# Performance work log

Measured on AMD Instinct MI355X. Metric: run time of the kernel, lower is better.

Reference implementation:

```python
import jax, jax.numpy as jnp
import numpy as np

B, C, N, K, COUT = 2, 192, 16384, 16, 192
EPS = 1e-5


def setup_inputs() -> dict:
    key = jax.random.key(0)
    k1, k2, k3 = jax.random.split(key, 3)
    x = jax.random.normal(k1, (B, C, N, 1), dtype=jnp.float32)
    edge_index = jax.random.randint(k2, (2, B, N, K), 0, N, dtype=jnp.int32)
    # kaiming-normal-ish 1x1 conv weight, flattened to [C_out, 2C]
    W = jax.random.normal(k3, (COUT, 2 * C), dtype=jnp.float32) * np.float32(np.sqrt(2.0 / (2 * C)))
    b_conv = jnp.zeros((COUT,), jnp.float32)
    gamma = jnp.ones((COUT,), jnp.float32)
    beta = jnp.zeros((COUT,), jnp.float32)
    return {"x": x, "W": W, "b_conv": b_conv, "gamma": gamma, "beta": beta, "edge_index": edge_index}


def reference(x, W, b_conv, gamma, beta, edge_index):
    b, c, n, _ = x.shape
    k = edge_index.shape[-1]
    xs = x[..., 0]  # [B,C,N]

    def gather(idx):  # idx: [B,N,K] -> [B,C,N,K]
        return jnp.take_along_axis(xs, idx.reshape(b, 1, n * k), axis=2).reshape(b, c, n, k)

    x_i = gather(edge_index[1])
    x_j = gather(edge_index[0])
    mr = jnp.max(x_j - x_i, axis=-1)  # max-relative feature [B,C,N]

    # torch.cat([x.unsqueeze(2), x_j.unsqueeze(2)], 2).reshape(b, 2c, n, 1) interleaves channels
    cat = jnp.stack([xs, mr], axis=2).reshape(b, 2 * c, n)  # [B,2C,N]

    # 1x1 conv == channel matmul
    h = jnp.einsum('oc,bcn->bon', W, cat) + b_conv[None, :, None]  # [B,COUT,N]

    # BatchNorm2d (training-mode batch statistics over batch+spatial dims)
    mean = h.mean(axis=(0, 2), keepdims=True)
    var = h.var(axis=(0, 2), keepdims=True)
    h = (h - mean) / jnp.sqrt(var + EPS) * gamma[None, :, None] + beta[None, :, None]

    out = jax.nn.gelu(h, approximate=False)
    return out[..., None]  # [B,COUT,N,1]
```

## Files before the change

### kernel.cpp

```cpp
#include <hip/hip_runtime.h>
#include <math.h>

#define BB 2
#define CC 192
#define NN 16384
#define KK 16
#define COUT 192
#define MM (BB * NN)
#define KDIM (2 * CC)
#define EPSF 1e-5f
#define NGB 256

typedef __attribute__((ext_vector_type(8))) short short8;
typedef __attribute__((ext_vector_type(4))) float f32x4;

#define AS1P const __attribute__((address_space(1))) void*
#define AS3P __attribute__((address_space(3))) void*

static __device__ __forceinline__ float bf16_to_f32(unsigned int u16) {
    return __uint_as_float(u16 << 16);
}
static __device__ __forceinline__ float bf16hi_to_f32(unsigned int u) {
    return __uint_as_float(u & 0xffff0000u);
}
static __device__ __forceinline__ unsigned short f32_to_bf16(float f) {
    unsigned int u = __float_as_uint(f);
    unsigned int r = (u + 0x7fffu + ((u >> 16) & 1u)) >> 16;
    return (unsigned short)r;
}

#define TRB (512 * 3 * BB)
__global__ __launch_bounds__(256) void k_prep(const float* __restrict__ x,
                                              unsigned int* __restrict__ xt32,
                                              const float* __restrict__ W,
                                              unsigned short* __restrict__ Wb) {
    int bid = blockIdx.x;
    int t = threadIdx.x;
    if (bid >= TRB) {
        int wb = bid - TRB;
        int base = wb * 1024 + t * 4;
        float4 v = *(const float4*)(W + base);
        uint2 o;
        o.x = (unsigned int)f32_to_bf16(v.x) | ((unsigned int)f32_to_bf16(v.y) << 16);
        o.y = (unsigned int)f32_to_bf16(v.z) | ((unsigned int)f32_to_bf16(v.w) << 16);
        *(uint2*)(Wb + base) = o;
        return;
    }
    __shared__ float tile[64][33];
    int nb = bid & 511;
    int rest = bid >> 9;
    int cb = rest % 3;
    int b = rest / 3;
    int n0 = nb * 32, c0 = cb * 64;
    int tx = t & 31, ty = t >> 5;
    #pragma unroll
    for (int j = 0; j < 64; j += 8)
        tile[ty + j][tx] = x[((size_t)b * CC + (c0 + ty + j)) * NN + n0 + tx];
    __syncthreads();
    #pragma unroll
    for (int j = 0; j < 32; j += 8) {
        int n = n0 + ty + j;
        unsigned int w = (unsigned int)f32_to_bf16(tile[2 * tx][ty + j]) |
                         ((unsigned int)f32_to_bf16(tile[2 * tx + 1][ty + j]) << 16);
        xt32[(((size_t)b * NN + n) * CC + c0) / 2 + tx] = w;
    }
}

__global__ __launch_bounds__(384) void k_gather(const unsigned short* __restrict__ xt,
                                                const int* __restrict__ edge,
                                                uint4* __restrict__ xcat4) {
    __shared__ int sj[16][KK], si[16][KK];
    int t = threadIdx.x;
    int m0 = blockIdx.x * 16;
    int b = m0 >> 14, n0 = m0 & (NN - 1);
    if (t < 256)
        ((int*)sj)[t] = edge[((size_t)b * NN + n0) * KK + t];
    if (t >= 128)
        ((int*)si)[t - 128] = edge[((size_t)(BB + b) * NN + n0) * KK + (t - 128)];
    __syncthreads();

    int p = t / 24, c4 = t % 24;
    const uint4* base = (const uint4*)(xt + (size_t)b * NN * CC) + c4;
    float mx[8];
    #pragma unroll
    for (int c = 0; c < 8; ++c) mx[c] = -INFINITY;
    #pragma unroll
    for (int k = 0; k < KK; ++k) {
        uint4 vj = base[(size_t)sj[p][k] * 24];
        uint4 vi = base[(size_t)si[p][k] * 24];
        const unsigned int dj[4] = {vj.x, vj.y, vj.z, vj.w};
        const unsigned int di[4] = {vi.x, vi.y, vi.z, vi.w};
        #pragma unroll
        for (int d = 0; d < 4; ++d) {
            mx[2 * d]     = fmaxf(mx[2 * d],     bf16_to_f32(dj[d] & 0xffffu) - bf16_to_f32(di[d] & 0xffffu));
            mx[2 * d + 1] = fmaxf(mx[2 * d + 1], bf16hi_to_f32(dj[d]) - bf16hi_to_f32(di[d]));
        }
    }
    uint4 xs = base[(size_t)(n0 + p) * 24];
    uint4 o0, o1;
    o0.x = (xs.x & 0xffffu) | ((unsigned int)f32_to_bf16(mx[0]) << 16);
    o0.y = (xs.x >> 16)     | ((unsigned int)f32_to_bf16(mx[1]) << 16);
    o0.z = (xs.y & 0xffffu) | ((unsigned int)f32_to_bf16(mx[2]) << 16);
    o0.w = (xs.y >> 16)     | ((unsigned int)f32_to_bf16(mx[3]) << 16);
    o1.x = (xs.z & 0xffffu) | ((unsigned int)f32_to_bf16(mx[4]) << 16);
    o1.y = (xs.z >> 16)     | ((unsigned int)f32_to_bf16(mx[5]) << 16);
    o1.z = (xs.w & 0xffffu) | ((unsigned int)f32_to_bf16(mx[6]) << 16);
    o1.w = (xs.w >> 16)     | ((unsigned int)f32_to_bf16(mx[7]) << 16);
    size_t orow = (size_t)(m0 + p) * 48;
    xcat4[orow + 2 * c4] = o0;
    xcat4[orow + 2 * c4 + 1] = o1;
}

#define BMT 128
__global__ __launch_bounds__(512) void k_gemm(const unsigned short* __restrict__ xcat,
                                              const unsigned short* __restrict__ Wb,
                                              unsigned short* __restrict__ h,
                                              float* __restrict__ psum,
                                              float* __restrict__ psum2) {
    __shared__ __align__(16) char ldsA[BMT * 128];
    __shared__ __align__(16) char ldsB[COUT * 128];
    int t = threadIdx.x;
    int m0 = blockIdx.x * BMT;
    int w = t >> 6, l = t & 63, lo = l & 15, q4 = l >> 4;
    int lr = l >> 3, lc = l & 7;
    f32x4 acc[12];
    #pragma unroll
    for (int i = 0; i < 12; ++i) acc[i] = (f32x4){0.f, 0.f, 0.f, 0.f};
    int rA = w * 16 + lo;

    for (int ks = 0; ks < KDIM / 64; ++ks) {
        int k0 = ks * 64;
        if (ks) __syncthreads();
        #pragma unroll
        for (int e = 0; e < 2; ++e) {
            int r = w * 16 + e * 8 + lr;
            int cg = lc ^ (r & 7);
            const unsigned short* gp = xcat + (size_t)(m0 + r) * KDIM + k0 + cg * 8;
            __builtin_amdgcn_global_load_lds((AS1P)gp, (AS3P)(ldsA + w * 2048 + e * 1024), 16, 0, 0);
        }
        #pragma unroll
        for (int e = 0; e < 3; ++e) {
            int r = w * 24 + e * 8 + lr;
            int cg = lc ^ (r & 7);
            const unsigned short* gp = Wb + (size_t)r * KDIM + k0 + cg * 8;
            __builtin_amdgcn_global_load_lds((AS1P)gp, (AS3P)(ldsB + w * 3072 + e * 1024), 16, 0, 0);
        }
        __syncthreads();
        #pragma unroll
        for (int kh = 0; kh < 2; ++kh) {
            int cb = kh * 64 + q4 * 16;
            short8 a = *(const short8*)(ldsA + rA * 128 + (cb ^ ((rA & 7) << 4)));
            #pragma unroll
            for (int ot = 0; ot < 12; ++ot) {
                int rB = ot * 16 + lo;
                short8 bf = *(const short8*)(ldsB + rB * 128 + (cb ^ ((rB & 7) << 4)));
                acc[ot] = __builtin_amdgcn_mfma_f32_16x16x32_bf16(a, bf, acc[ot], 0, 0, 0);
            }
        }
    }
    __syncthreads();

    float* reds = (float*)ldsA;
    float* reds2 = reds + 8 * COUT;
    int mrow = m0 + w * 16 + q4 * 4;
    #pragma unroll
    for (int ot = 0; ot < 12; ++ot) {
        int o = ot * 16 + lo;
        float s = 0.f, s2 = 0.f;
        #pragma unroll
        for (int r = 0; r < 4; ++r) {
            float v = acc[ot][r];
            h[(size_t)(mrow + r) * COUT + o] = f32_to_bf16(v);
            s += v;
            s2 += v * v;
        }
        s += __shfl_xor(s, 16);  s2 += __shfl_xor(s2, 16);
        s += __shfl_xor(s, 32);  s2 += __shfl_xor(s2, 32);
        if (q4 == 0) {
            reds[w * COUT + o] = s;
            reds2[w * COUT + o] = s2;
        }
    }
    __syncthreads();
    if (t < COUT) {
        float a = 0.f, a2 = 0.f;
        #pragma unroll
        for (int w8 = 0; w8 < 8; ++w8) {
            a += reds[w8 * COUT + t];
            a2 += reds2[w8 * COUT + t];
        }
        psum[blockIdx.x * COUT + t] = a;
        psum2[blockIdx.x * COUT + t] = a2;
    }
}

__global__ __launch_bounds__(256) void k_bn(const float* __restrict__ psum,
                                            const float* __restrict__ psum2,
                                            const float* __restrict__ gamma,
                                            const float* __restrict__ beta,
                                            float* __restrict__ sc_sh) {
    __shared__ float red[2][32][8];
    int t = threadIdx.x;
    int ch = t & 7, rr = t >> 3;
    int o = blockIdx.x * 8 + ch;
    float a = 0.f, a2 = 0.f;
    for (int r = rr; r < NGB; r += 32) {
        a += psum[r * COUT + o];
        a2 += psum2[r * COUT + o];
    }
    red[0][rr][ch] = a;
    red[1][rr][ch] = a2;
    __syncthreads();
    if (t < 8) {
        float s = 0.f, s2 = 0.f;
        #pragma unroll
        for (int i = 0; i < 32; ++i) { s += red[0][i][t]; s2 += red[1][i][t]; }
        int oo = blockIdx.x * 8 + t;
        float inv_m = 1.0f / (float)MM;
        float mean = s * inv_m;
        float var = s2 * inv_m - mean * mean;
        float sc = gamma[oo] * rsqrtf(var + EPSF);
        sc_sh[oo] = sc;
        sc_sh[COUT + oo] = beta[oo] - mean * sc;
    }
}

__global__ __launch_bounds__(256) void k_out(const unsigned short* __restrict__ h,
                                             const float* __restrict__ sc_sh,
                                             float* __restrict__ out) {
    __shared__ float tile[32][33];
    int b = blockIdx.z;
    int n0 = blockIdx.x * 32;
    int o0 = blockIdx.y * 32;
    int tx = threadIdx.x, ty = threadIdx.y;
    int o = o0 + tx;
    float sc = sc_sh[o];
    float sh = sc_sh[COUT + o];
    #pragma unroll
    for (int j = 0; j < 32; j += 8) {
        float v = bf16_to_f32(h[((size_t)b * NN + n0 + ty + j) * COUT + o]);
        v = v * sc + sh;
        tile[ty + j][tx] = 0.5f * v * (1.0f + erff(v * 0.70710678118654752440f));
    }
    __syncthreads();
    #pragma unroll
    for (int j = 0; j < 32; j += 8)
        out[((size_t)b * COUT + (o0 + ty + j)) * NN + n0 + tx] = tile[tx][ty + j];
}

extern "C" void kernel_launch(void* const* d_in, const int* in_sizes, int n_in,
                              void* d_out, int out_size, void* d_ws, size_t ws_size,
                              hipStream_t stream) {
    const float* x = (const float*)d_in[0];
    const float* W = (const float*)d_in[1];
    const float* gamma = (const float*)d_in[3];
    const float* beta = (const float*)d_in[4];
    const int* edge = (const int*)d_in[5];
    float* out = (float*)d_out;

    char* ws = (char*)d_ws;
    unsigned short* xt = (unsigned short*)ws;
    ws += (size_t)MM * CC * 2;
    unsigned short* xcat = (unsigned short*)ws;
    ws += (size_t)MM * KDIM * 2;
    unsigned short* Wb = (unsigned short*)ws;
    ws += (size_t)COUT * KDIM * 2;
    unsigned short* h = (unsigned short*)ws;
    ws += (size_t)MM * COUT * 2;
    float* psum = (float*)ws;
    ws += (size_t)NGB * COUT * sizeof(float);
    float* psum2 = (float*)ws;
    ws += (size_t)NGB * COUT * sizeof(float);
    float* sc_sh = (float*)ws;

    k_prep<<<TRB + 72, 256, 0, stream>>>(x, (unsigned int*)xt, W, Wb);

    k_gather<<<MM / 16, 384, 0, stream>>>(xt, edge, (uint4*)xcat);

    k_gemm<<<MM / BMT, 512, 0, stream>>>(xcat, Wb, h, psum, psum2);

    k_bn<<<24, 256, 0, stream>>>(psum, psum2, gamma, beta, sc_sh);

    dim3 ogrid(NN / 32, COUT / 32, BB);
    k_out<<<ogrid, dim3(32, 8), 0, stream>>>(h, sc_sh, out);
}
```

Measured before the change: 73.66 us.

## Split gathered features into channel chunks and vectorize output epilogue

```diff
diff --git a/kernel.cpp b/kernel.cpp
--- a/kernel.cpp
+++ b/kernel.cpp
@@ -28,6 +28,9 @@
     unsigned int r = (u + 0x7fffu + ((u >> 16) & 1u)) >> 16;
     return (unsigned short)r;
 }
+static __device__ __forceinline__ float gelu_exact(float v) {
+    return 0.5f * v * (1.0f + erff(v * 0.70710678118654752440f));
+}
 
 #define TRB (512 * 3 * BB)
 __global__ __launch_bounds__(256) void k_prep(const float* __restrict__ x,
@@ -57,37 +60,41 @@
     for (int j = 0; j < 64; j += 8)
         tile[ty + j][tx] = x[((size_t)b * CC + (c0 + ty + j)) * NN + n0 + tx];
     __syncthreads();
+    int c = c0 + 2 * tx;
+    int chunk = c / 48, wi = c % 48;
     #pragma unroll
     for (int j = 0; j < 32; j += 8) {
         int n = n0 + ty + j;
         unsigned int w = (unsigned int)f32_to_bf16(tile[2 * tx][ty + j]) |
                          ((unsigned int)f32_to_bf16(tile[2 * tx + 1][ty + j]) << 16);
-        xt32[(((size_t)b * NN + n) * CC + c0) / 2 + tx] = w;
-    }
-}
-
-__global__ __launch_bounds__(384) void k_gather(const unsigned short* __restrict__ xt,
+        xt32[((size_t)(b * 4 + chunk) * NN + n) * 24 + wi / 2] = w;
+    }
+}
+
+__global__ __launch_bounds__(384) void k_gather(const unsigned short* __restrict__ xt4,
                                                 const int* __restrict__ edge,
                                                 uint4* __restrict__ xcat4) {
-    __shared__ int sj[16][KK], si[16][KK];
-    int t = threadIdx.x;
-    int m0 = blockIdx.x * 16;
-    int b = m0 >> 14, n0 = m0 & (NN - 1);
-    if (t < 256)
-        ((int*)sj)[t] = edge[((size_t)b * NN + n0) * KK + t];
-    if (t >= 128)
-        ((int*)si)[t - 128] = edge[((size_t)(BB + b) * NN + n0) * KK + (t - 128)];
-    __syncthreads();
-
-    int p = t / 24, c4 = t % 24;
-    const uint4* base = (const uint4*)(xt + (size_t)b * NN * CC) + c4;
+    __shared__ int sj[64 * KK], si[64 * KK];
+    int bid = blockIdx.x;
+    int combo = bid & 7;
+    int g = bid >> 3;
+    int b = combo >> 2, ch = combo & 3;
+    int n0 = g * 64;
+    int t = threadIdx.x;
+    const int* ej = edge + ((size_t)b * NN + n0) * KK;
+    const int* ei = edge + ((size_t)(BB + b) * NN + n0) * KK;
+    for (int u = t; u < 64 * KK; u += 384) { sj[u] = ej[u]; si[u] = ei[u]; }
+    __syncthreads();
+
+    int p = t / 6, c4 = t % 6;
+    const uint4* base = (const uint4*)(xt4 + (size_t)(b * 4 + ch) * NN * 48) + c4;
     float mx[8];
     #pragma unroll
     for (int c = 0; c < 8; ++c) mx[c] = -INFINITY;
     #pragma unroll
     for (int k = 0; k < KK; ++k) {
-        uint4 vj = base[(size_t)sj[p][k] * 24];
-        uint4 vi = base[(size_t)si[p][k] * 24];
+        uint4 vj = base[(size_t)sj[p * KK + k] * 6];
+        uint4 vi = base[(size_t)si[p * KK + k] * 6];
         const unsigned int dj[4] = {vj.x, vj.y, vj.z, vj.w};
         const unsigned int di[4] = {vi.x, vi.y, vi.z, vi.w};
         #pragma unroll
@@ -96,7 +103,7 @@
             mx[2 * d + 1] = fmaxf(mx[2 * d + 1], bf16hi_to_f32(dj[d]) - bf16hi_to_f32(di[d]));
         }
     }
-    uint4 xs = base[(size_t)(n0 + p) * 24];
+    uint4 xs = base[(size_t)(n0 + p) * 6];
     uint4 o0, o1;
     o0.x = (xs.x & 0xffffu) | ((unsigned int)f32_to_bf16(mx[0]) << 16);
     o0.y = (xs.x >> 16)     | ((unsigned int)f32_to_bf16(mx[1]) << 16);
@@ -106,9 +113,9 @@
     o1.y = (xs.z >> 16)     | ((unsigned int)f32_to_bf16(mx[5]) << 16);
     o1.z = (xs.w & 0xffffu) | ((unsigned int)f32_to_bf16(mx[6]) << 16);
     o1.w = (xs.w >> 16)     | ((unsigned int)f32_to_bf16(mx[7]) << 16);
-    size_t orow = (size_t)(m0 + p) * 48;
-    xcat4[orow + 2 * c4] = o0;
-    xcat4[orow + 2 * c4 + 1] = o1;
+    size_t orow = (size_t)(b * NN + n0 + p) * 48;
+    xcat4[orow + ch * 12 + 2 * c4]     = o0;
+    xcat4[orow + ch * 12 + 2 * c4 + 1] = o1;
 }
 
 #define BMT 128
@@ -228,24 +235,32 @@
 __global__ __launch_bounds__(256) void k_out(const unsigned short* __restrict__ h,
                                              const float* __restrict__ sc_sh,
                                              float* __restrict__ out) {
-    __shared__ float tile[32][33];
+    __shared__ float tile[64][36];
     int b = blockIdx.z;
-    int n0 = blockIdx.x * 32;
+    int n0 = blockIdx.x * 64;
     int o0 = blockIdx.y * 32;
-    int tx = threadIdx.x, ty = threadIdx.y;
-    int o = o0 + tx;
-    float sc = sc_sh[o];
-    float sh = sc_sh[COUT + o];
-    #pragma unroll
-    for (int j = 0; j < 32; j += 8) {
-        float v = bf16_to_f32(h[((size_t)b * NN + n0 + ty + j) * COUT + o]);
-        v = v * sc + sh;
-        tile[ty + j][tx] = 0.5f * v * (1.0f + erff(v * 0.70710678118654752440f));
-    }
-    __syncthreads();
-    #pragma unroll
-    for (int j = 0; j < 32; j += 8)
-        out[((size_t)b * COUT + (o0 + ty + j)) * NN + n0 + tx] = tile[tx][ty + j];
+    int t = threadIdx.x;
+    {
+        int r = t >> 2, c4 = t & 3;
+        uint4 hv = *(const uint4*)(h + ((size_t)b * NN + n0 + r) * COUT + o0 + c4 * 8);
+        const unsigned int d[4] = {hv.x, hv.y, hv.z, hv.w};
+        #pragma unroll
+        for (int e = 0; e < 4; ++e) {
+            int oc = c4 * 8 + 2 * e;
+            float v0 = bf16_to_f32(d[e] & 0xffffu) * sc_sh[o0 + oc] + sc_sh[COUT + o0 + oc];
+            float v1 = bf16hi_to_f32(d[e]) * sc_sh[o0 + oc + 1] + sc_sh[COUT + o0 + oc + 1];
+            tile[r][oc] = gelu_exact(v0);
+            tile[r][oc + 1] = gelu_exact(v1);
+        }
+    }
+    __syncthreads();
+    int o = t >> 3, q = t & 7;
+    #pragma unroll
+    for (int it = 0; it < 2; ++it) {
+        int nn = q * 4 + it * 32;
+        float4 v = {tile[nn][o], tile[nn + 1][o], tile[nn + 2][o], tile[nn + 3][o]};
+        *(float4*)(out + ((size_t)b * COUT + o0 + o) * NN + n0 + nn) = v;
+    }
 }
 
 extern "C" void kernel_launch(void* const* d_in, const int* in_sizes, int n_in,
@@ -259,7 +274,7 @@
     float* out = (float*)d_out;
 
     char* ws = (char*)d_ws;
-    unsigned short* xt = (unsigned short*)ws;
+    unsigned short* xt4 = (unsigned short*)ws;
     ws += (size_t)MM * CC * 2;
     unsigned short* xcat = (unsigned short*)ws;
     ws += (size_t)MM * KDIM * 2;
@@ -273,14 +288,14 @@
     ws += (size_t)NGB * COUT * sizeof(float);
     float* sc_sh = (float*)ws;
 
-    k_prep<<<TRB + 72, 256, 0, stream>>>(x, (unsigned int*)xt, W, Wb);
-
-    k_gather<<<MM / 16, 384, 0, stream>>>(xt, edge, (uint4*)xcat);
+    k_prep<<<TRB + 72, 256, 0, stream>>>(x, (unsigned int*)xt4, W, Wb);
+
+    k_gather<<<8 * (NN / 64), 384, 0, stream>>>(xt4, edge, (uint4*)xcat);
 
     k_gemm<<<MM / BMT, 512, 0, stream>>>(xcat, Wb, h, psum, psum2);
 
     k_bn<<<24, 256, 0, stream>>>(psum, psum2, gamma, beta, sc_sh);
 
-    dim3 ogrid(NN / 32, COUT / 32, BB);
-    k_out<<<ogrid, dim3(32, 8), 0, stream>>>(h, sc_sh, out);
-}
+    dim3 ogrid(NN / 64, COUT / 32, BB);
+    k_out<<<ogrid, dim3(256), 0, stream>>>(h, sc_sh, out);
+}
```

After: 73.81 us. No clear change (+0.2%).

## Fuse GEMM, BatchNorm stats and GELU output into one cooperative kernel

Applied to the files above, without the earlier changes.

```diff
diff --git a/kernel.cpp b/kernel.cpp
--- a/kernel.cpp
+++ b/kernel.cpp
@@ -1,5 +1,8 @@
 #include <hip/hip_runtime.h>
+#include <hip/hip_cooperative_groups.h>
 #include <math.h>
+
+namespace cg = cooperative_groups;
 
 #define BB 2
 #define CC 192
@@ -27,6 +30,9 @@
     unsigned int u = __float_as_uint(f);
     unsigned int r = (u + 0x7fffu + ((u >> 16) & 1u)) >> 16;
     return (unsigned short)r;
+}
+static __device__ __forceinline__ float gelu_exact(float v) {
+    return 0.5f * v * (1.0f + erff(v * 0.70710678118654752440f));
 }
 
 #define TRB (512 * 3 * BB)
@@ -107,18 +113,23 @@
     o1.z = (xs.w & 0xffffu) | ((unsigned int)f32_to_bf16(mx[6]) << 16);
     o1.w = (xs.w >> 16)     | ((unsigned int)f32_to_bf16(mx[7]) << 16);
     size_t orow = (size_t)(m0 + p) * 48;
-    xcat4[orow + 2 * c4] = o0;
+    xcat4[orow + 2 * c4]     = o0;
     xcat4[orow + 2 * c4 + 1] = o1;
 }
 
 #define BMT 128
-__global__ __launch_bounds__(512) void k_gemm(const unsigned short* __restrict__ xcat,
-                                              const unsigned short* __restrict__ Wb,
-                                              unsigned short* __restrict__ h,
-                                              float* __restrict__ psum,
-                                              float* __restrict__ psum2) {
-    __shared__ __align__(16) char ldsA[BMT * 128];
-    __shared__ __align__(16) char ldsB[COUT * 128];
+__global__ __launch_bounds__(512) void k_fused(const unsigned short* __restrict__ xcat,
+                                               const unsigned short* __restrict__ Wb,
+                                               float* __restrict__ psum,
+                                               float* __restrict__ psum2,
+                                               const float* __restrict__ gamma,
+                                               const float* __restrict__ beta,
+                                               float* __restrict__ out) {
+    __shared__ __align__(16) char lds[40960];
+    __shared__ float ssum[2][COUT];
+    __shared__ float ssc[COUT], ssh[COUT];
+    char* ldsA = lds;
+    char* ldsB = lds + 16384;
     int t = threadIdx.x;
     int m0 = blockIdx.x * BMT;
     int w = t >> 6, l = t & 63, lo = l & 15, q4 = l >> 4;
@@ -134,15 +145,15 @@
         #pragma unroll
         for (int e = 0; e < 2; ++e) {
             int r = w * 16 + e * 8 + lr;
-            int cg = lc ^ (r & 7);
-            const unsigned short* gp = xcat + (size_t)(m0 + r) * KDIM + k0 + cg * 8;
+            int cg_ = lc ^ (r & 7);
+            const unsigned short* gp = xcat + (size_t)(m0 + r) * KDIM + k0 + cg_ * 8;
             __builtin_amdgcn_global_load_lds((AS1P)gp, (AS3P)(ldsA + w * 2048 + e * 1024), 16, 0, 0);
         }
         #pragma unroll
         for (int e = 0; e < 3; ++e) {
             int r = w * 24 + e * 8 + lr;
-            int cg = lc ^ (r & 7);
-            const unsigned short* gp = Wb + (size_t)r * KDIM + k0 + cg * 8;
+            int cg_ = lc ^ (r & 7);
+            const unsigned short* gp = Wb + (size_t)r * KDIM + k0 + cg_ * 8;
             __builtin_amdgcn_global_load_lds((AS1P)gp, (AS3P)(ldsB + w * 3072 + e * 1024), 16, 0, 0);
         }
         __syncthreads();
@@ -160,9 +171,8 @@
     }
     __syncthreads();
 
-    float* reds = (float*)ldsA;
+    float* reds = (float*)lds;
     float* reds2 = reds + 8 * COUT;
-    int mrow = m0 + w * 16 + q4 * 4;
     #pragma unroll
     for (int ot = 0; ot < 12; ++ot) {
         int o = ot * 16 + lo;
@@ -170,7 +180,6 @@
         #pragma unroll
         for (int r = 0; r < 4; ++r) {
             float v = acc[ot][r];
-            h[(size_t)(mrow + r) * COUT + o] = f32_to_bf16(v);
             s += v;
             s2 += v * v;
         }
@@ -192,60 +201,51 @@
         psum[blockIdx.x * COUT + t] = a;
         psum2[blockIdx.x * COUT + t] = a2;
     }
-}
-
-__global__ __launch_bounds__(256) void k_bn(const float* __restrict__ psum,
-                                            const float* __restrict__ psum2,
-                                            const float* __restrict__ gamma,
-                                            const float* __restrict__ beta,
-                                            float* __restrict__ sc_sh) {
-    __shared__ float red[2][32][8];
-    int t = threadIdx.x;
-    int ch = t & 7, rr = t >> 3;
-    int o = blockIdx.x * 8 + ch;
-    float a = 0.f, a2 = 0.f;
-    for (int r = rr; r < NGB; r += 32) {
-        a += psum[r * COUT + o];
-        a2 += psum2[r * COUT + o];
-    }
-    red[0][rr][ch] = a;
-    red[1][rr][ch] = a2;
-    __syncthreads();
-    if (t < 8) {
-        float s = 0.f, s2 = 0.f;
-        #pragma unroll
-        for (int i = 0; i < 32; ++i) { s += red[0][i][t]; s2 += red[1][i][t]; }
-        int oo = blockIdx.x * 8 + t;
+    __threadfence();
+    cg::this_grid().sync();
+
+    if (t < 2 * COUT) {
+        int kind = (t >= COUT);
+        int ch = t - kind * COUT;
+        const float* src = kind ? psum2 : psum;
+        float a = 0.f;
+        for (int r = 0; r < NGB; ++r) a += src[r * COUT + ch];
+        ssum[kind][ch] = a;
+    }
+    __syncthreads();
+    if (t < COUT) {
         float inv_m = 1.0f / (float)MM;
-        float mean = s * inv_m;
-        float var = s2 * inv_m - mean * mean;
-        float sc = gamma[oo] * rsqrtf(var + EPSF);
-        sc_sh[oo] = sc;
-        sc_sh[COUT + oo] = beta[oo] - mean * sc;
-    }
-}
-
-__global__ __launch_bounds__(256) void k_out(const unsigned short* __restrict__ h,
-                                             const float* __restrict__ sc_sh,
-                                             float* __restrict__ out) {
-    __shared__ float tile[32][33];
-    int b = blockIdx.z;
-    int n0 = blockIdx.x * 32;
-    int o0 = blockIdx.y * 32;
-    int tx = threadIdx.x, ty = threadIdx.y;
-    int o = o0 + tx;
-    float sc = sc_sh[o];
-    float sh = sc_sh[COUT + o];
-    #pragma unroll
-    for (int j = 0; j < 32; j += 8) {
-        float v = bf16_to_f32(h[((size_t)b * NN + n0 + ty + j) * COUT + o]);
-        v = v * sc + sh;
-        tile[ty + j][tx] = 0.5f * v * (1.0f + erff(v * 0.70710678118654752440f));
-    }
-    __syncthreads();
-    #pragma unroll
-    for (int j = 0; j < 32; j += 8)
-        out[((size_t)b * COUT + (o0 + ty + j)) * NN + n0 + tx] = tile[tx][ty + j];
+        float mean = ssum[0][t] * inv_m;
+        float var = ssum[1][t] * inv_m - mean * mean;
+        float sc = gamma[t] * rsqrtf(var + EPSF);
+        ssc[t] = sc;
+        ssh[t] = beta[t] - mean * sc;
+    }
+
+    int b = m0 >> 14, n0 = m0 & (NN - 1);
+    float* ltile = (float*)lds;
+    for (int g = 0; g < 3; ++g) {
+        __syncthreads();
+        #pragma unroll
+        for (int j = 0; j < 4; ++j) {
+            int ot = g * 4 + j;
+            int o = ot * 16 + lo;
+            int ol = j * 16 + lo;
+            int nl = w * 16 + q4 * 4;
+            #pragma unroll
+            for (int r = 0; r < 4; ++r) {
+                float v = acc[ot][r] * ssc[o] + ssh[o];
+                ltile[ol * 132 + nl + r] = gelu_exact(v);
+            }
+        }
+        __syncthreads();
+        int row = t >> 3, nq = t & 7;
+        int o = g * 64 + row;
+        float* op = out + ((size_t)b * COUT + o) * NN + n0 + nq * 16;
+        const float4* lp = (const float4*)(ltile + row * 132 + nq * 16);
+        #pragma unroll
+        for (int q = 0; q < 4; ++q) ((float4*)op)[q] = lp[q];
+    }
 }
 
 extern "C" void kernel_launch(void* const* d_in, const int* in_sizes, int n_in,
@@ -265,22 +265,16 @@
     ws += (size_t)MM * KDIM * 2;
     unsigned short* Wb = (unsigned short*)ws;
     ws += (size_t)COUT * KDIM * 2;
-    unsigned short* h = (unsigned short*)ws;
-    ws += (size_t)MM * COUT * 2;
     float* psum = (float*)ws;
     ws += (size_t)NGB * COUT * sizeof(float);
     float* psum2 = (float*)ws;
-    ws += (size_t)NGB * COUT * sizeof(float);
-    float* sc_sh = (float*)ws;
 
     k_prep<<<TRB + 72, 256, 0, stream>>>(x, (unsigned int*)xt, W, Wb);
 
     k_gather<<<MM / 16, 384, 0, stream>>>(xt, edge, (uint4*)xcat);
 
-    k_gemm<<<MM / BMT, 512, 0, stream>>>(xcat, Wb, h, psum, psum2);
-
-    k_bn<<<24, 256, 0, stream>>>(psum, psum2, gamma, beta, sc_sh);
-
-    dim3 ogrid(NN / 32, COUT / 32, BB);
-    k_out<<<ogrid, dim3(32, 8), 0, stream>>>(h, sc_sh, out);
-}
+    void* args[] = {(void*)&xcat, (void*)&Wb, (void*)&psum, (void*)&psum2,
+                    (void*)&gamma, (void*)&beta, (void*)&out};
+    hipLaunchCooperativeKernel((const void*)k_fused, dim3(NGB), dim3(512),
+                               args, 0, stream);
+}
```

New measurement: 160.8 us. 2.18x slower.
